# Kernel optimization log

Measured on AMD Instinct MI355X. Metric: run time of the kernel, lower is better.

Reference implementation:

```python
import jax, jax.numpy as jnp
import numpy as np

B, LQ, LKV = 4, 512, 8192
Q_DIM, KV_DIM = 1024, 512
QK_CH, V_CH, N_HEADS = 256, 256, 8
EPS = 1e-5


def _layernorm(x, g, b):
    m = jnp.mean(x, axis=-1, keepdims=True)
    v = jnp.mean(jnp.square(x - m), axis=-1, keepdims=True)
    return (x - m) * jax.lax.rsqrt(v + EPS) * g + b


def setup_inputs() -> dict:
    key = jax.random.key(0)
    ks = jax.random.split(key, 8)
    hidden_states = jax.random.normal(ks[0], (B, LQ, Q_DIM), dtype=jnp.float32)
    inputs = jax.random.normal(ks[1], (B, LKV, KV_DIM), dtype=jnp.float32)
    # Linear weights stored as [in, out] for x @ W
    Wq = jax.random.normal(ks[2], (Q_DIM, QK_CH), dtype=jnp.float32) * (1.0 / np.sqrt(Q_DIM))
    Wk = jax.random.normal(ks[3], (KV_DIM, QK_CH), dtype=jnp.float32) * (1.0 / np.sqrt(KV_DIM))
    Wv = jax.random.normal(ks[4], (KV_DIM, V_CH), dtype=jnp.float32) * (1.0 / np.sqrt(KV_DIM))
    bq = jnp.zeros((QK_CH,), jnp.float32)
    bk = jax.random.normal(ks[5], (QK_CH,), dtype=jnp.float32) * 0.02
    bv = jax.random.normal(ks[6], (V_CH,), dtype=jnp.float32) * 0.02
    ln1_g = jnp.ones((Q_DIM,), jnp.float32)
    ln1_b = jnp.zeros((Q_DIM,), jnp.float32)
    ln2_g = jnp.ones((KV_DIM,), jnp.float32)
    ln2_b = jnp.zeros((KV_DIM,), jnp.float32)
    return dict(hidden_states=hidden_states, inputs=inputs,
                ln1_g=ln1_g, ln1_b=ln1_b, ln2_g=ln2_g, ln2_b=ln2_b,
                Wq=Wq, bq=bq, Wk=Wk, bk=bk, Wv=Wv, bv=bv)


def reference(hidden_states, inputs, ln1_g, ln1_b, ln2_g, ln2_b,
              Wq, bq, Wk, bk, Wv, bv):
    H = N_HEADS
    dqk = QK_CH // H
    dv = V_CH // H
    hs = _layernorm(hidden_states, ln1_g, ln1_b)          # [B,LQ,Q_DIM]
    inp = _layernorm(inputs, ln2_g, ln2_b)                # [B,LKV,KV_DIM]
    q = (hs @ Wq + bq).reshape(B, LQ, H, dqk)             # [B,LQ,H,dqk]
    k = (inp @ Wk + bk).reshape(B, LKV, H, dqk)           # [B,LKV,H,dqk]
    v = (inp @ Wv + bv).reshape(B, LKV, H, dv)            # [B,LKV,H,dv]
    scores = jnp.einsum('bqhd,bkhd->bhqk', q, k) / np.sqrt(dqk).astype(np.float32)
    probs = jax.nn.softmax(scores, axis=-1)               # [B,H,LQ,LKV] (materialized, as in torch)
    ctx = jnp.einsum('bhqk,bkhd->bqhd', probs, v)         # [B,LQ,H,dv]
    return ctx.reshape(B, LQ, H * dv)
```

## Files before the change

kernel.cpp:

```cpp
#include <hip/hip_runtime.h>
#include <hip/hip_bf16.h>
#include <math.h>

#define NB    4
#define LQ    512
#define LKV   8192
#define QDIM  1024
#define KVDIM 512
#define NH    8
#define EPS_LN 1e-5f
#define SMAX  12.0f

typedef __attribute__((ext_vector_type(8))) short bf16x8;
typedef __attribute__((ext_vector_type(4))) float f32x4;

static __device__ __forceinline__ ushort f2bf(float x) {
    unsigned int u = __builtin_bit_cast(unsigned int, x);
    u += 0x7FFFu + ((u >> 16) & 1u);
    return (ushort)(u >> 16);
}

#if __has_builtin(__builtin_amdgcn_cvt_pk_bf16_f32)
static __device__ __forceinline__ unsigned int pk_bf16(float a, float b) {
    auto r = __builtin_amdgcn_cvt_pk_bf16_f32(a, b);
    return __builtin_bit_cast(unsigned int, r);
}
#else
static __device__ __forceinline__ unsigned int pk_bf16(float a, float b) {
    return (unsigned int)f2bf(a) | ((unsigned int)f2bf(b) << 16);
}
#endif

#if __has_builtin(__builtin_amdgcn_exp2f)
#define EXP2F(x) __builtin_amdgcn_exp2f(x)
#else
#define EXP2F(x) exp2f(x)
#endif

static __device__ __forceinline__ void gld_lds16(const ushort* g, ushort* l) {
    __builtin_amdgcn_global_load_lds(
        (const __attribute__((address_space(1))) unsigned int*)g,
        (__attribute__((address_space(3))) unsigned int*)l, 16, 0, 0);
}

template<int K>
static __device__ __forceinline__ void ln_norm_row(
    const float* __restrict__ x, const float* __restrict__ g,
    const float* __restrict__ bta, ushort* __restrict__ y, int row, int lane)
{
    const float* xp = x + (size_t)row * K;
    constexpr int NV = K / 256;
    float4 v[NV];
    float s = 0.f;
#pragma unroll
    for (int i = 0; i < NV; ++i) {
        v[i] = *(const float4*)(xp + lane * 4 + i * 256);
        s += v[i].x + v[i].y + v[i].z + v[i].w;
    }
#pragma unroll
    for (int o = 1; o < 64; o <<= 1) s += __shfl_xor(s, o, 64);
    const float mu = s * (1.0f / K);
    float vs = 0.f;
#pragma unroll
    for (int i = 0; i < NV; ++i) {
        float dx = v[i].x - mu, dy = v[i].y - mu, dz = v[i].z - mu, dw = v[i].w - mu;
        vs += dx * dx + dy * dy + dz * dz + dw * dw;
    }
#pragma unroll
    for (int o = 1; o < 64; o <<= 1) vs += __shfl_xor(vs, o, 64);
    const float rs = rsqrtf(vs * (1.0f / K) + EPS_LN);
#pragma unroll
    for (int i = 0; i < NV; ++i) {
        const float4 gv = *(const float4*)(g   + lane * 4 + i * 256);
        const float4 bv = *(const float4*)(bta + lane * 4 + i * 256);
        uint2 o;
        o.x = pk_bf16((v[i].x - mu) * rs * gv.x + bv.x, (v[i].y - mu) * rs * gv.y + bv.y);
        o.y = pk_bf16((v[i].z - mu) * rs * gv.z + bv.z, (v[i].w - mu) * rs * gv.w + bv.w);
        *(uint2*)(y + (size_t)row * K + lane * 4 + i * 256) = o;
    }
}

static __device__ __forceinline__ void ln_stats_row(
    const float* __restrict__ x, float* __restrict__ mean, float* __restrict__ rstd,
    int row, int lane)
{
    const float* xp = x + (size_t)row * QDIM;
    float4 v[4];
    float s = 0.f;
#pragma unroll
    for (int i = 0; i < 4; ++i) {
        v[i] = *(const float4*)(xp + lane * 4 + i * 256);
        s += v[i].x + v[i].y + v[i].z + v[i].w;
    }
#pragma unroll
    for (int o = 1; o < 64; o <<= 1) s += __shfl_xor(s, o, 64);
    const float mu = s * (1.0f / QDIM);
    float vs = 0.f;
#pragma unroll
    for (int i = 0; i < 4; ++i) {
        float dx = v[i].x - mu, dy = v[i].y - mu, dz = v[i].z - mu, dw = v[i].w - mu;
        vs += dx * dx + dy * dy + dz * dz + dw * dw;
    }
#pragma unroll
    for (int o = 1; o < 64; o <<= 1) vs += __shfl_xor(vs, o, 64);
    if (lane == 0) {
        mean[row] = mu;
        rstd[row] = rsqrtf(vs * (1.0f / QDIM) + EPS_LN);
    }
}

static __device__ __forceinline__ void wt_transpose_body(
    const float* __restrict__ src, ushort* __restrict__ dst, int K,
    int kx, int ny, int t, ushort (*Ts)[72])
{
    const int k0 = kx * 64, n0 = ny * 64;
    const int nl = t & 63;
#pragma unroll
    for (int p = 0; p < 16; ++p) {
        const int kl = p * 4 + (t >> 6);
        Ts[nl][kl] = f2bf(src[(size_t)(k0 + kl) * 256 + n0 + nl]);
    }
    __syncthreads();
    const int ck = (t & 7) * 8;
#pragma unroll
    for (int p = 0; p < 2; ++p) {
        const int rn = p * 32 + (t >> 3);
        *(bf16x8*)(dst + (size_t)(n0 + rn) * K + k0 + ck) = *(const bf16x8*)&Ts[rn][ck];
    }
}

__global__ __launch_bounds__(256) void phaseA_kernel(
    const float* __restrict__ inputs, const float* __restrict__ ln2g,
    const float* __restrict__ ln2b,   ushort* __restrict__ Abf,
    const float* __restrict__ hidden, float* __restrict__ mean_h, float* __restrict__ rstd_h,
    const float* __restrict__ Wq, const float* __restrict__ Wk, const float* __restrict__ Wv,
    ushort* __restrict__ WtQ, ushort* __restrict__ WtKV)
{
    __shared__ ushort Ts[64][72];
    const int bid = blockIdx.x;
    const int t = threadIdx.x;
    const int lane = t & 63;
    if (bid < 8192) {
        ln_norm_row<KVDIM>(inputs, ln2g, ln2b, Abf, bid * 4 + (t >> 6), lane);
    } else if (bid < 8704) {
        ln_stats_row(hidden, mean_h, rstd_h, (bid - 8192) * 4 + (t >> 6), lane);
    } else if (bid < 8768) {
        const int p = bid - 8704;
        wt_transpose_body(Wq, WtQ, QDIM, p & 15, p >> 4, t, Ts);
    } else if (bid < 8800) {
        const int p = bid - 8768;
        wt_transpose_body(Wk, WtKV, KVDIM, p & 7, p >> 3, t, Ts);
    } else {
        const int p = bid - 8800;
        wt_transpose_body(Wv, WtKV + (size_t)256 * KVDIM, KVDIM, p & 7, p >> 3, t, Ts);
    }
}

__global__ __launch_bounds__(256) void phaseB_kernel(
    const ushort* __restrict__ Abf, const ushort* __restrict__ WtKV,
    const float* __restrict__ bk, const float* __restrict__ bv,
    ushort* __restrict__ kb, ushort* __restrict__ vt,
    const float* __restrict__ hidden, const float* __restrict__ mean_h,
    const float* __restrict__ rstd_h,
    const float* __restrict__ ln1g, const float* __restrict__ ln1b,
    const ushort* __restrict__ WtQ, const float* __restrict__ bq,
    ushort* __restrict__ qb, float oscale)
{
    __shared__ __align__(16) ushort SMEM[4 * 64 * 72];
    const int bid  = blockIdx.x;
    const int t    = threadIdx.x;
    const int lane = t & 63;
    const int w    = t >> 6;
    const int lq   = lane & 15;
    const int lg   = lane >> 4;
    const int wm   = w >> 1;
    const int wn   = w & 1;

    if (bid < 1024) {
        const int bm = (bid >> 2) * 128;
        const int bn = (bid & 3) * 128;
        ushort* As = SMEM;
        ushort* Bs = SMEM + 4096;

        const int srow = t >> 2;
        const int scol = ((t & 3) ^ ((t >> 3) & 3)) * 8;
        const ushort* gA = Abf  + (size_t)(bm + srow) * KVDIM + scol;
        const ushort* gB = WtKV + (size_t)(bn + srow) * KVDIM + scol;
        ushort* lA = As + t * 8;
        ushort* lB = Bs + t * 8;

        f32x4 acc[4][4] = {};
        for (int k0 = 0; k0 < KVDIM; k0 += 32) {
            gld_lds16(gA + k0,                       lA);
            gld_lds16(gA + (size_t)64 * KVDIM + k0,  lA + 2048);
            gld_lds16(gB + k0,                       lB);
            gld_lds16(gB + (size_t)64 * KVDIM + k0,  lB + 2048);
            __syncthreads();
            bf16x8 af[4], bf[4];
#pragma unroll
            for (int mt = 0; mt < 4; ++mt) {
                const int m = wm * 64 + mt * 16 + lq;
                af[mt] = *(const bf16x8*)(As + m * 32 + ((lg ^ ((m >> 1) & 3)) << 3));
            }
#pragma unroll
            for (int nt = 0; nt < 4; ++nt) {
                const int n = wn * 64 + nt * 16 + lq;
                bf[nt] = *(const bf16x8*)(Bs + n * 32 + ((lg ^ ((n >> 1) & 3)) << 3));
            }
#pragma unroll
            for (int mt = 0; mt < 4; ++mt)
#pragma unroll
                for (int nt = 0; nt < 4; ++nt)
                    acc[mt][nt] = __builtin_amdgcn_mfma_f32_16x16x32_bf16(af[mt], bf[nt], acc[mt][nt], 0, 0, 0);
            __syncthreads();
        }
        const int m0base = bm + wm * 64;
        const int bidx   = m0base >> 13;
        const int tokb   = m0base & 8191;

        if (bn < 256) {
            ushort (*Cs)[72] = (ushort(*)[72])(SMEM + w * 64 * 72);
#pragma unroll
            for (int nt = 0; nt < 4; ++nt) {
                const int n_l = nt * 16 + lq;
                const float bias = bk[bn + wn * 64 + n_l];
#pragma unroll
                for (int mt = 0; mt < 4; ++mt)
#pragma unroll
                    for (int r = 0; r < 4; ++r)
                        Cs[mt * 16 + lg * 4 + r][n_l] = f2bf(acc[mt][nt][r] + bias);
            }
            const int r0 = lane >> 3;
            const int ck = (lane & 7) * 8;
            const int nc = bn + wn * 64 + ck;
            const int h = nc >> 5, d = nc & 31;
            const size_t obase = (((size_t)(bidx * NH + h) << 13) + tokb) * 32 + d;
#pragma unroll
            for (int p = 0; p < 8; ++p) {
                const int row = p * 8 + r0;
                *(bf16x8*)(kb + obase + (size_t)row * 32) = *(const bf16x8*)&Cs[row][ck];
            }
        } else {
            ushort (*Cs)[72] = (ushort(*)[72])(SMEM + w * 64 * 72);
#pragma unroll
            for (int nt = 0; nt < 4; ++nt) {
                const int n_l = nt * 16 + lq;
                const float bias = bv[(bn - 256) + wn * 64 + n_l];
#pragma unroll
                for (int mt = 0; mt < 4; ++mt) {
                    uint2 o;
                    o.x = pk_bf16(acc[mt][nt][0] + bias, acc[mt][nt][1] + bias);
                    o.y = pk_bf16(acc[mt][nt][2] + bias, acc[mt][nt][3] + bias);
                    *(uint2*)&Cs[n_l][mt * 16 + lg * 4] = o;
                }
            }
            const int r0 = lane >> 3;
            const int cm = (lane & 7) * 8;
            const int tokc = tokb + cm;
#pragma unroll
            for (int p = 0; p < 8; ++p) {
                const int row = p * 8 + r0;
                const int nv  = (bn - 256) + wn * 64 + row;
                const int h = nv >> 5, d = nv & 31;
                *(bf16x8*)(vt + ((size_t)(bidx * NH + h) * 32 + d) * LKV + tokc) =
                    *(const bf16x8*)&Cs[row][cm];
            }
        }
    } else {
        const int p  = bid - 1024;
        const int bm = (p >> 2) * 64;
        const int bn = (p & 3) * 64;
        ushort* As = SMEM;
        ushort* Bs = SMEM + 4096;

        const int srow = t >> 3;
        const int scol = ((t & 7) ^ (srow & 7)) * 8;
        const ushort* gB = WtQ + (size_t)(bn + srow) * QDIM + scol;
        ushort* lB  = Bs + t * 8;
        ushort* lA0 = As + t * 8;
        ushort* lA1 = As + 2048 + t * 8;

        const int r0 = bm + srow;
        const float mu0 = mean_h[r0],      rs0 = rstd_h[r0];
        const float mu1 = mean_h[r0 + 32], rs1 = rstd_h[r0 + 32];
        const float* xA0 = hidden + (size_t)r0 * QDIM + scol;
        const float* xA1 = xA0 + (size_t)32 * QDIM;

        f32x4 acc[2][2] = {};
        for (int k0 = 0; k0 < QDIM; k0 += 64) {
            gld_lds16(gB + k0,                      lB);
            gld_lds16(gB + (size_t)32 * QDIM + k0,  lB + 2048);
            const float4 a0 = *(const float4*)(xA0 + k0);
            const float4 a1 = *(const float4*)(xA0 + k0 + 4);
            const float4 c0 = *(const float4*)(xA1 + k0);
            const float4 c1 = *(const float4*)(xA1 + k0 + 4);
            const float4 g0 = *(const float4*)(ln1g + k0 + scol);
            const float4 g1 = *(const float4*)(ln1g + k0 + scol + 4);
            const float4 d0 = *(const float4*)(ln1b + k0 + scol);
            const float4 d1 = *(const float4*)(ln1b + k0 + scol + 4);
            uint4 w0, w1;
            w0.x = pk_bf16((a0.x - mu0) * rs0 * g0.x + d0.x, (a0.y - mu0) * rs0 * g0.y + d0.y);
            w0.y = pk_bf16((a0.z - mu0) * rs0 * g0.z + d0.z, (a0.w - mu0) * rs0 * g0.w + d0.w);
            w0.z = pk_bf16((a1.x - mu0) * rs0 * g1.x + d1.x, (a1.y - mu0) * rs0 * g1.y + d1.y);
            w0.w = pk_bf16((a1.z - mu0) * rs0 * g1.z + d1.z, (a1.w - mu0) * rs0 * g1.w + d1.w);
            w1.x = pk_bf16((c0.x - mu1) * rs1 * g0.x + d0.x, (c0.y - mu1) * rs1 * g0.y + d0.y);
            w1.y = pk_bf16((c0.z - mu1) * rs1 * g0.z + d0.z, (c0.w - mu1) * rs1 * g0.w + d0.w);
            w1.z = pk_bf16((c1.x - mu1) * rs1 * g1.x + d1.x, (c1.y - mu1) * rs1 * g1.y + d1.y);
            w1.w = pk_bf16((c1.z - mu1) * rs1 * g1.z + d1.z, (c1.w - mu1) * rs1 * g1.w + d1.w);
            *(uint4*)lA0 = w0;
            *(uint4*)lA1 = w1;
            __syncthreads();
#pragma unroll
            for (int kh = 0; kh < 2; ++kh) {
                bf16x8 af[2], bf[2];
#pragma unroll
                for (int mt = 0; mt < 2; ++mt) {
                    const int m = wm * 32 + mt * 16 + lq;
                    af[mt] = *(const bf16x8*)(As + m * 64 + (((lg + 4 * kh) ^ (m & 7)) << 3));
                }
#pragma unroll
                for (int nt = 0; nt < 2; ++nt) {
                    const int n = wn * 32 + nt * 16 + lq;
                    bf[nt] = *(const bf16x8*)(Bs + n * 64 + (((lg + 4 * kh) ^ (n & 7)) << 3));
                }
#pragma unroll
                for (int mt = 0; mt < 2; ++mt)
#pragma unroll
                    for (int nt = 0; nt < 2; ++nt)
                        acc[mt][nt] = __builtin_amdgcn_mfma_f32_16x16x32_bf16(af[mt], bf[nt], acc[mt][nt], 0, 0, 0);
            }
            __syncthreads();
        }

#pragma unroll
        for (int nt = 0; nt < 2; ++nt) {
            const int n = bn + wn * 32 + nt * 16 + lq;
            const int h = n >> 5, d = n & 31;
            const float bias = bq[n];
#pragma unroll
            for (int mt = 0; mt < 2; ++mt) {
                const int m0   = bm + wm * 32 + mt * 16 + lg * 4;
                const int bidx = m0 >> 9;
                const int tok  = m0 & 511;
                const size_t base = (((size_t)(bidx * NH + h) << 9) + tok) * 32 + d;
#pragma unroll
                for (int r = 0; r < 4; ++r)
                    qb[base + (size_t)r * 32] = f2bf((acc[mt][nt][r] + bias) * oscale);
            }
        }
    }
}

__global__ __launch_bounds__(512, 4) void attn_mfma_kernel(
    const ushort* __restrict__ Qb,
    const ushort* __restrict__ Kb,
    const ushort* __restrict__ Vt,
    float* __restrict__ Out)
{
    const int bid = blockIdx.x;
    const int xcd = bid & 7;
    const int rr  = bid >> 3;
    const int bh  = ((rr & 3) << 3) | xcd;
    const int qt  = rr >> 2;
    const int b = bh >> 3, h = bh & 7;
    const int t = threadIdx.x, w = t >> 6, lane = t & 63;
    const int lq = lane & 15, lg = lane >> 4;

    __shared__ __align__(16) ushort Pb[2][8][32][72];
    __shared__ float lbuf[8][32];

    bf16x8 qfrag[2];
    const size_t qbase = ((size_t)bh * LQ + qt * 32) * 32;
    qfrag[0] = *(const bf16x8*)(Qb + qbase + (size_t)lq * 32 + lg * 8);
    qfrag[1] = *(const bf16x8*)(Qb + qbase + (size_t)(16 + lq) * 32 + lg * 8);

    const ushort* KpA = Kb + ((size_t)bh * LKV + w * 1024 + lq) * 32 + lg * 8;
    const ushort* VpA = Vt + ((size_t)bh * 32 + lq) * LKV + w * 1024 + lg * 8;

    f32x4 oacc[2][2] = {};
    float l_part[2] = {0.f, 0.f};
    const f32x4 cM = {-SMAX, -SMAX, -SMAX, -SMAX};

    bf16x8 kf[4], vf[2][2];
#pragma unroll
    for (int m = 0; m < 4; ++m)
        kf[m] = *(const bf16x8*)(KpA + (size_t)(m * 16) * 32);
#pragma unroll
    for (int dt = 0; dt < 2; ++dt)
#pragma unroll
        for (int hf = 0; hf < 2; ++hf)
            vf[dt][hf] = *(const bf16x8*)(VpA + (size_t)(dt * 16) * LKV + hf * 32);

    for (int kt = 0; kt < 1024; kt += 64) {
        bf16x8 kc[4], vc[2][2];
#pragma unroll
        for (int m = 0; m < 4; ++m) kc[m] = kf[m];
#pragma unroll
        for (int dt = 0; dt < 2; ++dt)
#pragma unroll
            for (int hf = 0; hf < 2; ++hf) vc[dt][hf] = vf[dt][hf];

        const int nk = (kt + 64 < 1024) ? kt + 64 : 0;
#pragma unroll
        for (int m = 0; m < 4; ++m)
            kf[m] = *(const bf16x8*)(KpA + (size_t)(nk + m * 16) * 32);
#pragma unroll
        for (int dt = 0; dt < 2; ++dt)
#pragma unroll
            for (int hf = 0; hf < 2; ++hf)
                vf[dt][hf] = *(const bf16x8*)(VpA + (size_t)(dt * 16) * LKV + nk + hf * 32);

        f32x4 s[4][2];
#pragma unroll
        for (int m = 0; m < 4; ++m)
#pragma unroll
            for (int n = 0; n < 2; ++n)
                s[m][n] = __builtin_amdgcn_mfma_f32_16x16x32_bf16(kc[m], qfrag[n], cM, 0, 0, 0);

        ushort* myP = &Pb[(kt >> 6) & 1][w][0][0];

#pragma unroll
        for (int n = 0; n < 2; ++n) {
#pragma unroll
            for (int m = 0; m < 4; ++m) {
                const float p0 = EXP2F(s[m][n][0]);
                const float p1 = EXP2F(s[m][n][1]);
                const float p2 = EXP2F(s[m][n][2]);
                const float p3 = EXP2F(s[m][n][3]);
                l_part[n] += ((p0 + p1) + (p2 + p3));
                uint2 pw;
                pw.x = pk_bf16(p0, p1);
                pw.y = pk_bf16(p2, p3);
                *(uint2*)(myP + (n * 16 + lq) * 72 + m * 16 + lg * 4) = pw;
            }
        }

        bf16x8 pf[2][2];
#pragma unroll
        for (int n = 0; n < 2; ++n)
#pragma unroll
            for (int hf = 0; hf < 2; ++hf)
                pf[n][hf] = *(const bf16x8*)(myP + (size_t)(n * 16 + lq) * 72 + hf * 32 + lg * 8);

#pragma unroll
        for (int dt = 0; dt < 2; ++dt)
#pragma unroll
            for (int n = 0; n < 2; ++n) {
                oacc[dt][n] = __builtin_amdgcn_mfma_f32_16x16x32_bf16(vc[dt][0], pf[n][0], oacc[dt][n], 0, 0, 0);
                oacc[dt][n] = __builtin_amdgcn_mfma_f32_16x16x32_bf16(vc[dt][1], pf[n][1], oacc[dt][n], 0, 0, 0);
            }
    }

#pragma unroll
    for (int n = 0; n < 2; ++n) {
        l_part[n] += __shfl_xor(l_part[n], 16);
        l_part[n] += __shfl_xor(l_part[n], 32);
    }
    if (lg == 0) {
        lbuf[w][lq]      = l_part[0];
        lbuf[w][16 + lq] = l_part[1];
    }
    __syncthreads();

    float* Ob = (float*)&Pb[0][0][0][0];
    if (w >= 4) {
#pragma unroll
        for (int n = 0; n < 2; ++n)
#pragma unroll
            for (int dt = 0; dt < 2; ++dt)
                *(f32x4*)&Ob[((size_t)(w - 4) * 32 + n * 16 + lq) * 36 + dt * 16 + lg * 4] = oacc[dt][n];
    }
    __syncthreads();
    if (w < 4) {
#pragma unroll
        for (int n = 0; n < 2; ++n)
#pragma unroll
            for (int dt = 0; dt < 2; ++dt) {
                float* p = &Ob[((size_t)w * 32 + n * 16 + lq) * 36 + dt * 16 + lg * 4];
                f32x4 v = *(f32x4*)p;
                v += oacc[dt][n];
                *(f32x4*)p = v;
            }
    }
    __syncthreads();
    {
        const int q  = t >> 4;
        const int d0 = (t & 15) * 2;
        float s0 = 0.f, s1 = 0.f;
#pragma unroll
        for (int j = 0; j < 4; ++j) {
            s0 += Ob[((size_t)j * 32 + q) * 36 + d0];
            s1 += Ob[((size_t)j * 32 + q) * 36 + d0 + 1];
        }
        float gl = 0.f;
#pragma unroll
        for (int j = 0; j < 8; ++j) gl += lbuf[j][q];
        const float inv = 1.0f / gl;
        float2 o; o.x = s0 * inv; o.y = s1 * inv;
        *(float2*)(Out + ((size_t)b * LQ + qt * 32 + q) * 256 + h * 32 + d0) = o;
    }
}

extern "C" void kernel_launch(void* const* d_in, const int* in_sizes, int n_in,
                              void* d_out, int out_size, void* d_ws, size_t ws_size,
                              hipStream_t stream)
{
    const float* hidden = (const float*)d_in[0];
    const float* inputs = (const float*)d_in[1];
    const float* ln1g   = (const float*)d_in[2];
    const float* ln1b   = (const float*)d_in[3];
    const float* ln2g   = (const float*)d_in[4];
    const float* ln2b   = (const float*)d_in[5];
    const float* Wq     = (const float*)d_in[6];
    const float* bq     = (const float*)d_in[7];
    const float* Wk     = (const float*)d_in[8];
    const float* bk     = (const float*)d_in[9];
    const float* Wv     = (const float*)d_in[10];
    const float* bv     = (const float*)d_in[11];
    float* out = (float*)d_out;

    char* wsb = (char*)d_ws;
    ushort* qb     = (ushort*)(wsb);
    ushort* WtKV   = (ushort*)(wsb + (1u << 20));
    ushort* WtQ    = (ushort*)(wsb + (1u << 20) + (512u << 10));
    float*  mean_h = (float*)(wsb + (2u << 20));
    float*  rstd_h = (float*)(wsb + (2u << 20) + 8192);
    ushort* kb     = (ushort*)(wsb + (2u << 20) + 16384);
    ushort* vt     = (ushort*)(wsb + (18u << 20) + 16384);
    ushort* Abf    = (ushort*)(wsb + (34u << 20) + 16384);

    const float oscale = 0.2550540226496112f;

    phaseA_kernel<<<8832, 256, 0, stream>>>(inputs, ln2g, ln2b, Abf,
                                            hidden, mean_h, rstd_h,
                                            Wq, Wk, Wv, WtQ, WtKV);
    phaseB_kernel<<<1152, 256, 0, stream>>>(Abf, WtKV, bk, bv, kb, vt,
                                            hidden, mean_h, rstd_h, ln1g, ln1b,
                                            WtQ, bq, qb, oscale);
    attn_mfma_kernel<<<512, 512, 0, stream>>>(qb, kb, vt, out);
}
```

Baseline: 216.8 us.

## Keep P in registers using 16x16x16 MFMA layout, drop LDS round-trip

```diff
diff --git a/kernel.cpp b/kernel.cpp
--- a/kernel.cpp
+++ b/kernel.cpp
@@ -12,6 +12,7 @@
 #define SMAX  12.0f
 
 typedef __attribute__((ext_vector_type(8))) short bf16x8;
+typedef __attribute__((ext_vector_type(4))) short bf16x4;
 typedef __attribute__((ext_vector_type(4))) float f32x4;
 
 static __device__ __forceinline__ ushort f2bf(float x) {
@@ -35,6 +36,18 @@
 #define EXP2F(x) __builtin_amdgcn_exp2f(x)
 #else
 #define EXP2F(x) exp2f(x)
+#endif
+
+#if __has_builtin(__builtin_amdgcn_mfma_f32_16x16x16bf16_1k)
+static __device__ __forceinline__ f32x4 mfma16(bf16x4 a, bf16x4 b, f32x4 c) {
+    return __builtin_amdgcn_mfma_f32_16x16x16bf16_1k(a, b, c, 0, 0, 0);
+}
+#else
+static __device__ __forceinline__ f32x4 mfma16(bf16x4 a, bf16x4 b, f32x4 c) {
+    f32x4 d;
+    asm("v_mfma_f32_16x16x16_bf16 %0, %1, %2, %3" : "=v"(d) : "v"(a), "v"(b), "v"(c));
+    return d;
+}
 #endif
 
 static __device__ __forceinline__ void gld_lds16(const ushort* g, ushort* l) {
@@ -351,6 +364,53 @@
     }
 }
 
+static __device__ __forceinline__ void attn_step(
+    bf16x4 (&kc)[4][2], bf16x4 (&kn)[4][2], const bf16x4 (&qf)[2][2],
+    const ushort* __restrict__ Kp, const ushort* __restrict__ Vp0,
+    const ushort* __restrict__ Vp1,
+    int kt, f32x4 (&oacc)[2][2], float (&l_part)[2], const f32x4 cM)
+{
+    bf16x4 vf[2][4];
+#pragma unroll
+    for (int m = 0; m < 4; ++m) {
+        vf[0][m] = *(const bf16x4*)(Vp0 + kt + m * 16);
+        vf[1][m] = *(const bf16x4*)(Vp1 + kt + m * 16);
+    }
+    const int nk = (kt + 64 < 1024) ? kt + 64 : 0;
+#pragma unroll
+    for (int m = 0; m < 4; ++m) {
+        kn[m][0] = *(const bf16x4*)(Kp + (size_t)(nk + m * 16) * 32);
+        kn[m][1] = *(const bf16x4*)(Kp + (size_t)(nk + m * 16) * 32 + 16);
+    }
+    bf16x4 pf[2][4];
+#pragma unroll
+    for (int n = 0; n < 2; ++n) {
+#pragma unroll
+        for (int m = 0; m < 4; ++m) {
+            f32x4 s = mfma16(kc[m][0], qf[n][0], cM);
+            s = mfma16(kc[m][1], qf[n][1], s);
+            const float p0 = EXP2F(s[0]);
+            const float p1 = EXP2F(s[1]);
+            const float p2 = EXP2F(s[2]);
+            const float p3 = EXP2F(s[3]);
+            l_part[n] += ((p0 + p1) + (p2 + p3));
+            uint2 pw;
+            pw.x = pk_bf16(p0, p1);
+            pw.y = pk_bf16(p2, p3);
+            pf[n][m] = __builtin_bit_cast(bf16x4, pw);
+        }
+    }
+#pragma unroll
+    for (int dt = 0; dt < 2; ++dt)
+#pragma unroll
+        for (int n = 0; n < 2; ++n) {
+            oacc[dt][n] = mfma16(vf[dt][0], pf[n][0], oacc[dt][n]);
+            oacc[dt][n] = mfma16(vf[dt][1], pf[n][1], oacc[dt][n]);
+            oacc[dt][n] = mfma16(vf[dt][2], pf[n][2], oacc[dt][n]);
+            oacc[dt][n] = mfma16(vf[dt][3], pf[n][3], oacc[dt][n]);
+        }
+}
+
 __global__ __launch_bounds__(512, 4) void attn_mfma_kernel(
     const ushort* __restrict__ Qb,
     const ushort* __restrict__ Kb,
@@ -366,89 +426,35 @@
     const int t = threadIdx.x, w = t >> 6, lane = t & 63;
     const int lq = lane & 15, lg = lane >> 4;
 
-    __shared__ __align__(16) ushort Pb[2][8][32][72];
+    __shared__ __align__(16) float Ob[4 * 32 * 36];
     __shared__ float lbuf[8][32];
 
-    bf16x8 qfrag[2];
+    bf16x4 qf[2][2];
     const size_t qbase = ((size_t)bh * LQ + qt * 32) * 32;
-    qfrag[0] = *(const bf16x8*)(Qb + qbase + (size_t)lq * 32 + lg * 8);
-    qfrag[1] = *(const bf16x8*)(Qb + qbase + (size_t)(16 + lq) * 32 + lg * 8);
-
-    const ushort* KpA = Kb + ((size_t)bh * LKV + w * 1024 + lq) * 32 + lg * 8;
-    const ushort* VpA = Vt + ((size_t)bh * 32 + lq) * LKV + w * 1024 + lg * 8;
+#pragma unroll
+    for (int n = 0; n < 2; ++n) {
+        qf[n][0] = *(const bf16x4*)(Qb + qbase + (size_t)(n * 16 + lq) * 32 + lg * 4);
+        qf[n][1] = *(const bf16x4*)(Qb + qbase + (size_t)(n * 16 + lq) * 32 + 16 + lg * 4);
+    }
+
+    const ushort* Kp  = Kb + ((size_t)bh * LKV + w * 1024 + lq) * 32 + lg * 4;
+    const ushort* Vp0 = Vt + ((size_t)bh * 32 + lq) * LKV + w * 1024 + lg * 4;
+    const ushort* Vp1 = Vp0 + (size_t)16 * LKV;
 
     f32x4 oacc[2][2] = {};
     float l_part[2] = {0.f, 0.f};
     const f32x4 cM = {-SMAX, -SMAX, -SMAX, -SMAX};
 
-    bf16x8 kf[4], vf[2][2];
-#pragma unroll
-    for (int m = 0; m < 4; ++m)
-        kf[m] = *(const bf16x8*)(KpA + (size_t)(m * 16) * 32);
-#pragma unroll
-    for (int dt = 0; dt < 2; ++dt)
-#pragma unroll
-        for (int hf = 0; hf < 2; ++hf)
-            vf[dt][hf] = *(const bf16x8*)(VpA + (size_t)(dt * 16) * LKV + hf * 32);
-
-    for (int kt = 0; kt < 1024; kt += 64) {
-        bf16x8 kc[4], vc[2][2];
-#pragma unroll
-        for (int m = 0; m < 4; ++m) kc[m] = kf[m];
-#pragma unroll
-        for (int dt = 0; dt < 2; ++dt)
-#pragma unroll
-            for (int hf = 0; hf < 2; ++hf) vc[dt][hf] = vf[dt][hf];
-
-        const int nk = (kt + 64 < 1024) ? kt + 64 : 0;
-#pragma unroll
-        for (int m = 0; m < 4; ++m)
-            kf[m] = *(const bf16x8*)(KpA + (size_t)(nk + m * 16) * 32);
-#pragma unroll
-        for (int dt = 0; dt < 2; ++dt)
-#pragma unroll
-            for (int hf = 0; hf < 2; ++hf)
-                vf[dt][hf] = *(const bf16x8*)(VpA + (size_t)(dt * 16) * LKV + nk + hf * 32);
-
-        f32x4 s[4][2];
-#pragma unroll
-        for (int m = 0; m < 4; ++m)
-#pragma unroll
-            for (int n = 0; n < 2; ++n)
-                s[m][n] = __builtin_amdgcn_mfma_f32_16x16x32_bf16(kc[m], qfrag[n], cM, 0, 0, 0);
-
-        ushort* myP = &Pb[(kt >> 6) & 1][w][0][0];
-
-#pragma unroll
-        for (int n = 0; n < 2; ++n) {
-#pragma unroll
-            for (int m = 0; m < 4; ++m) {
-                const float p0 = EXP2F(s[m][n][0]);
-                const float p1 = EXP2F(s[m][n][1]);
-                const float p2 = EXP2F(s[m][n][2]);
-                const float p3 = EXP2F(s[m][n][3]);
-                l_part[n] += ((p0 + p1) + (p2 + p3));
-                uint2 pw;
-                pw.x = pk_bf16(p0, p1);
-                pw.y = pk_bf16(p2, p3);
-                *(uint2*)(myP + (n * 16 + lq) * 72 + m * 16 + lg * 4) = pw;
-            }
-        }
-
-        bf16x8 pf[2][2];
-#pragma unroll
-        for (int n = 0; n < 2; ++n)
-#pragma unroll
-            for (int hf = 0; hf < 2; ++hf)
-                pf[n][hf] = *(const bf16x8*)(myP + (size_t)(n * 16 + lq) * 72 + hf * 32 + lg * 8);
-
-#pragma unroll
-        for (int dt = 0; dt < 2; ++dt)
-#pragma unroll
-            for (int n = 0; n < 2; ++n) {
-                oacc[dt][n] = __builtin_amdgcn_mfma_f32_16x16x32_bf16(vc[dt][0], pf[n][0], oacc[dt][n], 0, 0, 0);
-                oacc[dt][n] = __builtin_amdgcn_mfma_f32_16x16x32_bf16(vc[dt][1], pf[n][1], oacc[dt][n], 0, 0, 0);
-            }
+    bf16x4 kA[4][2], kB[4][2];
+#pragma unroll
+    for (int m = 0; m < 4; ++m) {
+        kA[m][0] = *(const bf16x4*)(Kp + (size_t)(m * 16) * 32);
+        kA[m][1] = *(const bf16x4*)(Kp + (size_t)(m * 16) * 32 + 16);
+    }
+
+    for (int kt = 0; kt < 1024; kt += 128) {
+        attn_step(kA, kB, qf, Kp, Vp0, Vp1, kt,      oacc, l_part, cM);
+        attn_step(kB, kA, qf, Kp, Vp0, Vp1, kt + 64, oacc, l_part, cM);
     }
 
 #pragma unroll
@@ -460,9 +466,6 @@
         lbuf[w][lq]      = l_part[0];
         lbuf[w][16 + lq] = l_part[1];
     }
-    __syncthreads();
-
-    float* Ob = (float*)&Pb[0][0][0][0];
     if (w >= 4) {
 #pragma unroll
         for (int n = 0; n < 2; ++n)
```

Measured after the change: 255.1 us. +17.7%, slower.
